# Performance work log

Measured on AMD Instinct MI355X. Metric: run time of the kernel, lower is better.

Reference implementation:

```python
import jax, jax.numpy as jnp
import numpy as np

B, D_IN, M, D_MEM = 65536, 64, 2048, 64


def setup_inputs() -> dict:
    key = jax.random.key(0)
    k = jax.random.split(key, 5)
    glorot = lambda kk, shape: jax.random.uniform(
        kk, shape, jnp.float32,
        -jnp.sqrt(6.0 / (shape[0] + shape[1])), jnp.sqrt(6.0 / (shape[0] + shape[1])))
    return {
        "inputs": jax.random.normal(k[0], (B, D_IN), jnp.float32),
        "W_att": glorot(k[1], (D_IN, M)),
        "b_att": jnp.zeros((M,), jnp.float32),
        "W_write": glorot(k[2], (D_IN, D_MEM)),
        "b_write": jnp.zeros((D_MEM,), jnp.float32),
        "memory": glorot(k[3], (M, D_MEM)),
        "update_gate": jnp.full((M,), 0.5, jnp.float32),
    }


def reference(inputs, W_att, b_att, W_write, b_write, memory, update_gate):
    # Read attention: Dense(memory_size, softmax) -> [B, M]
    read_attention = jax.nn.softmax(inputs @ W_att + b_att, axis=-1)
    # Read: [B, M] @ [M, Dm] -> [B, Dm]
    read_vector = read_attention @ memory
    # Write candidate: Dense(memory_dim, tanh) -> [B, Dm]
    candidate_write = jnp.tanh(inputs @ W_write + b_write)
    aggregated_write = jnp.mean(candidate_write, axis=0)[None, :]  # [1, Dm]
    write_attention = jnp.mean(read_attention, axis=0)             # [M]
    update_weights = (write_attention * update_gate)[:, None]      # [M, 1]
    # Gated in-place memory update (returned as new state)
    new_memory = memory * (1.0 - update_weights) + update_weights * aggregated_write
    return read_vector, new_memory
```

## Files before the change

### kernel.cpp

```cpp
#include <hip/hip_runtime.h>
#include <hip/hip_bf16.h>

typedef unsigned int   u32;
typedef unsigned short u16;

typedef __bf16 bf16x8 __attribute__((ext_vector_type(8)));
typedef float  f32x4  __attribute__((ext_vector_type(4)));
typedef u32    u32x4  __attribute__((ext_vector_type(4)));
typedef u32    u32x2  __attribute__((ext_vector_type(2)));

union Frag { u32x4 u; bf16x8 b; };

#define MFMA16 __builtin_amdgcn_mfma_f32_16x16x32_bf16

#define B_ROWS 65536
#define D_IN   64
#define M_SZ   2048
#define D_MEM  64

#define WT_OFF      0
#define MEMT_OFF    262144
#define WWT_OFF     524288
#define CSF_OFF     532480
#define AGF_OFF     540672
#define BATTS_OFF   540928

#define L2E 1.4426950408889634f

#define AS1 __attribute__((address_space(1)))
#define AS3 __attribute__((address_space(3)))

#if defined(__has_builtin)
#if __has_builtin(__builtin_amdgcn_global_load_lds)
#define HAS_GLD 1
#endif
#endif
#ifndef HAS_GLD
#define HAS_GLD 0
#endif

__device__ __forceinline__ float bf2f(u16 h) { return __uint_as_float(((u32)h) << 16); }
__device__ __forceinline__ u16 f2bf(float f) {
    u32 u = __float_as_uint(f);
    return (u16)((u + 0x7FFFu + ((u >> 16) & 1u)) >> 16);
}
#if defined(__has_builtin) && __has_builtin(__builtin_amdgcn_exp2f)
__device__ __forceinline__ float exp2fast(float x) { return __builtin_amdgcn_exp2f(x); }
#else
__device__ __forceinline__ float exp2fast(float x) { return __expf(x * 0.6931471805599453f); }
#endif
__device__ __forceinline__ float tanh_fast(float x) {
    const float e = exp2fast(x * (2.0f * L2E));
    return 1.0f - 2.0f * __builtin_amdgcn_rcpf(e + 1.0f);
}
__device__ __forceinline__ bool detect_bf16(const void* ug) {
    return ((const u32*)ug)[0] == 0x3F003F00u;
}
__device__ __forceinline__ float load_elem(const void* p, size_t i, bool isbf) {
    return isbf ? bf2f(((const u16*)p)[i]) : ((const float*)p)[i];
}

__device__ __forceinline__ u32 cvtpk_bf16(float lo, float hi) {
    u32 r;
    asm("v_cvt_pk_bf16_f32 %0, %1, %2" : "=v"(r) : "v"(lo), "v"(hi));
    return r;
}
#if defined(__has_builtin) && __has_builtin(__builtin_amdgcn_permlane32_swap) && \
    __has_builtin(__builtin_amdgcn_permlane16_swap)
__device__ __forceinline__ void pl32swap(u32& a, u32& b) {
    u32x2 r = __builtin_amdgcn_permlane32_swap(a, b, false, false);
    a = r[0]; b = r[1];
}
__device__ __forceinline__ void pl16swap(u32& a, u32& b) {
    u32x2 r = __builtin_amdgcn_permlane16_swap(a, b, false, false);
    a = r[0]; b = r[1];
}
#else
__device__ __forceinline__ void pl32swap(u32& a, u32& b) {
    asm("v_permlane32_swap_b32 %0, %1" : "+v"(a), "+v"(b));
}
__device__ __forceinline__ void pl16swap(u32& a, u32& b) {
    asm("v_permlane16_swap_b32 %0, %1" : "+v"(a), "+v"(b));
}
#endif
template<int CTRL>
__device__ __forceinline__ float xadd(float v) {
    int x = __builtin_amdgcn_update_dpp(0, __float_as_int(v), CTRL, 0xF, 0xF, true);
    return v + __int_as_float(x);
}

__global__ void __launch_bounds__(256)
prep_kernel(const void* Watt, const void* mem_in, const void* Wwr,
            const void* batt_in, const void* ug,
            u16* Wt, u16* memT, u16* Wwt, float* CSF, float* battS)
{
    const bool isbf = detect_bf16(ug);
    const int b = blockIdx.x;
    const int t = threadIdx.x;
    if (b == 65) {
        for (int i = t; i < 2112; i += 256) CSF[i] = 0.f;
        for (int i = t; i < 2048; i += 256)
            battS[i] = load_elem(batt_in, i, isbf) * L2E;
        return;
    }
    __shared__ u16 tile[64][65];
    const void* src; u16* dst; int C, rb, cb, bsel;
    if (b < 32)      { src = Watt;   dst = Wt;   C = 2048; rb = 0;           cb = b * 64; bsel = 0; }
    else if (b < 64) { src = mem_in; dst = memT; C = 64;   rb = (b-32) * 64; cb = 0;      bsel = 1; }
    else             { src = Wwr;    dst = Wwt;  C = 64;   rb = 0;           cb = 0;      bsel = 2; }

#pragma unroll
    for (int j = 0; j < 16; ++j) {
        int e = j * 256 + t;
        int r = e >> 6, c = e & 63;
        float v = load_elem(src, (size_t)(rb + r) * C + cb + c, isbf);
        tile[r][c] = f2bf(v);
    }
    __syncthreads();
#pragma unroll
    for (int j = 0; j < 16; ++j) {
        int e = j * 256 + t;
        int c2 = e >> 6, r2 = e & 63;
        size_t di;
        if (bsel == 0) {
            const int m = cb + c2;
            const int k2 = (r2 & 7) | ((((r2 >> 3) ^ m) & 7) << 3);
            di = (size_t)m * 64 + k2;
        } else if (bsel == 1) {
            const int m2 = (r2 & 7) | ((((r2 >> 3) ^ c2) & 7) << 3);
            di = (size_t)c2 * 2048 + rb + m2;
        } else {
            di = (size_t)c2 * 64 + r2;
        }
        dst[di] = tile[r2][c2];
    }
}

__global__ void __launch_bounds__(512, 4)
main_kernel(const void* x_in, const void* bwrite_in,
            const u16* __restrict__ Wt, const u16* __restrict__ memT,
            const u16* __restrict__ Wwt, const float* __restrict__ battS,
            const void* ug, float* CSF, float* AGF, void* out)
{
    const bool isbf = detect_bf16(ug);
    const int tid = threadIdx.x;
    const int lane = tid & 63, wave = tid >> 6;
    const int quad = lane >> 4, l4 = lane & 15;
    const int rowbase = blockIdx.x * 128;

    __shared__ __align__(16) u16 WtA[2][8192];
    __shared__ __align__(16) u16 MeL[2][64][128];
    __shared__ float csA[2112];

    const int wvu = __builtin_amdgcn_readfirstlane(wave);

    for (int i = tid; i < 2112; i += 512) csA[i] = 0.f;

    auto cp16 = [&](const char* gsrc_lane, char* lds_base_uniform) {
#if HAS_GLD
        __builtin_amdgcn_global_load_lds((const AS1 void*)gsrc_lane,
                                         (AS3 void*)lds_base_uniform, 16, 0, 0);
#else
        *(u32x4*)(lds_base_uniform + lane * 16) = *(const u32x4*)gsrc_lane;
#endif
    };
    auto stageWt = [&](int ch, int b) {
        char* lb = (char*)&WtA[b][0] + wvu * 2048;
        const char* gb = (const char*)Wt + (size_t)ch * 16384 + wvu * 2048 + lane * 16;
        cp16(gb, lb);
        cp16(gb + 1024, lb + 1024);
    };
    auto stageMe = [&](int ch, int b) {
#pragma unroll
        for (int j = 0; j < 2; ++j) {
            const int d = wvu * 8 + j * 4 + (lane >> 4);
            const char* gb = (const char*)memT + (size_t)d * 4096
                           + (size_t)ch * 256 + (lane & 15) * 16;
            char* lb = (char*)&MeL[b][wvu * 8 + j * 4][0];
            cp16(gb, lb);
        }
    };

    Frag a[2];
    {
        const int arow = rowbase + wave * 16 + l4;
        if (isbf) {
            const u16* xp = (const u16*)x_in + (size_t)arow * 64 + quad * 8;
            a[0].u = *(const u32x4*)xp;
            a[1].u = *(const u32x4*)(xp + 32);
        } else {
            const float* xp = (const float*)x_in + (size_t)arow * 64 + quad * 8;
#pragma unroll
            for (int j = 0; j < 8; ++j) {
                ((u16*)&a[0])[j] = f2bf(xp[j]);
                ((u16*)&a[1])[j] = f2bf(xp[32 + j]);
            }
        }
    }
    const f32x4 zf = {0.f, 0.f, 0.f, 0.f};

    stageWt(0, 0);

    float agout = 0.f;
    {
        f32x4 accW[4];
#pragma unroll
        for (int t = 0; t < 4; ++t) {
            const u16* bp = Wwt + (size_t)(t * 16 + l4) * 64 + quad * 8;
            Frag b0, b1; b0.u = *(const u32x4*)bp; b1.u = *(const u32x4*)(bp + 32);
            accW[t] = MFMA16(a[0].b, b0.b, zf, 0, 0, 0);
            accW[t] = MFMA16(a[1].b, b1.b, accW[t], 0, 0, 0);
        }
#pragma unroll
        for (int t = 0; t < 4; ++t) {
            const float bw = load_elem(bwrite_in, t * 16 + l4, isbf);
            float s = 0.f;
#pragma unroll
            for (int i = 0; i < 4; ++i) s += tanh_fast(accW[t][i] + bw);
            s += __shfl_xor(s, 16, 64);
            s += __shfl_xor(s, 32, 64);
            if (quad == t) agout = s;
        }
    }

    __syncthreads();
    atomicAdd(&csA[2048 + lane], agout);

    float lsum = 0.f;
    for (int ch = 0; ch < 16; ++ch) {
        const int cur = ch & 1;
        if (ch < 15) stageWt(ch + 1, cur ^ 1);
        for (int half = 0; half < 2; ++half) {
            const int mb = half * 64;
            const int mbase = ch * 128 + mb;
            Frag wb0[4], wb1[4]; f32x4 blv[4];
#pragma unroll
            for (int t = 0; t < 4; ++t) {
                const int rr = mb + t * 16 + l4, swr = rr & 7;
                wb0[t].u = *(const u32x4*)&WtA[cur][rr * 64 + ((quad ^ swr) << 3)];
                wb1[t].u = *(const u32x4*)&WtA[cur][rr * 64 + (((quad + 4) ^ swr) << 3)];
                blv[t] = *(const f32x4*)&battS[mbase + t * 16 + quad * 4];
            }
#pragma unroll
            for (int t = 0; t < 4; ++t) {
                f32x4 acc = MFMA16(wb0[t].b, a[0].b, zf, 0, 0, 0);
                acc = MFMA16(wb1[t].b, a[1].b, acc, 0, 0, 0);
#pragma unroll
                for (int i = 0; i < 4; ++i)
                    lsum += exp2fast(fmaf(acc[i], L2E, blv[t][i]));
            }
        }
        __syncthreads();
    }
    float invl;
    {
        float v = lsum;
        v += __shfl_xor(v, 16, 64);
        v += __shfl_xor(v, 32, 64);
        invl = 1.f / v;
    }

    f32x4 oaccT[4] = {zf, zf, zf, zf};
    stageMe(15, 1);
    __syncthreads();
    const bool sb0 = (l4 & 1), sb1 = (l4 & 2), sb2 = (l4 & 4), sb3 = (l4 & 8);
    for (int ch = 15; ch >= 0; --ch) {
        const int cur = ch & 1;
        if (ch > 0) { stageWt(ch - 1, cur ^ 1); stageMe(ch - 1, cur ^ 1); }
        for (int half = 0; half < 2; ++half) {
            const int mb = half * 64;
            const int mbase = ch * 128 + mb;
            const int mbh8 = mb >> 3;
            Frag wb0[4], wb1[4], mb0[4], mb1[4]; f32x4 blv[4];
#pragma unroll
            for (int t = 0; t < 4; ++t) {
                const int rr = mb + t * 16 + l4, swr = rr & 7;
                wb0[t].u = *(const u32x4*)&WtA[cur][rr * 64 + ((quad ^ swr) << 3)];
                wb1[t].u = *(const u32x4*)&WtA[cur][rr * 64 + (((quad + 4) ^ swr) << 3)];
                const int dd = t * 16 + l4, swd = dd & 7;
                mb0[t].u = *(const u32x4*)&MeL[cur][dd][(mbh8 | (quad ^ swd)) << 3];
                mb1[t].u = *(const u32x4*)&MeL[cur][dd][(mbh8 | ((quad + 4) ^ swd)) << 3];
                blv[t] = *(const f32x4*)&battS[mbase + t * 16 + quad * 4];
            }
            u32 P0[4], P1[4];
            float c16[16];
#pragma unroll
            for (int j = 0; j < 16; ++j) c16[j] = 0.f;
#pragma unroll
            for (int t = 0; t < 4; ++t) {
                f32x4 acc = MFMA16(wb0[t].b, a[0].b, zf, 0, 0, 0);
                acc = MFMA16(wb1[t].b, a[1].b, acc, 0, 0, 0);
                const float e0 = exp2fast(fmaf(acc[0], L2E, blv[t][0]));
                const float e1 = exp2fast(fmaf(acc[1], L2E, blv[t][1]));
                const float e2 = exp2fast(fmaf(acc[2], L2E, blv[t][2]));
                const float e3 = exp2fast(fmaf(acc[3], L2E, blv[t][3]));
                c16[t * 4 + 0] = fmaf(e0, invl, c16[t * 4 + 0]);
                c16[t * 4 + 1] = fmaf(e1, invl, c16[t * 4 + 1]);
                c16[t * 4 + 2] = fmaf(e2, invl, c16[t * 4 + 2]);
                c16[t * 4 + 3] = fmaf(e3, invl, c16[t * 4 + 3]);
                P0[t] = cvtpk_bf16(e0, e1);
                P1[t] = cvtpk_bf16(e2, e3);
            }
#pragma unroll
            for (int cc2 = 0; cc2 < 2; ++cc2) {
                u32 b0 = P0[2 * cc2], b2 = P0[2 * cc2 + 1];
                u32 b1 = P1[2 * cc2], b3 = P1[2 * cc2 + 1];
                pl32swap(b0, b2); pl16swap(b0, b2);
                pl32swap(b1, b3); pl16swap(b1, b3);
                Frag bf; bf.u = (u32x4){b0, b1, b2, b3};
#pragma unroll
                for (int dt = 0; dt < 4; ++dt) {
                    if (cc2 == 0)
                        oaccT[dt] = MFMA16(mb0[dt].b, bf.b, oaccT[dt], 0, 0, 0);
                    else
                        oaccT[dt] = MFMA16(mb1[dt].b, bf.b, oaccT[dt], 0, 0, 0);
                }
            }
            float u8[8];
#pragma unroll
            for (int k = 0; k < 8; ++k) {
                const float t0 = xadd<0xB1>(c16[2 * k]);
                const float t1 = xadd<0xB1>(c16[2 * k + 1]);
                u8[k] = sb0 ? t1 : t0;
            }
            float v4[4];
#pragma unroll
            for (int k = 0; k < 4; ++k) {
                const float t0 = xadd<0x4E>(u8[2 * k]);
                const float t1 = xadd<0x4E>(u8[2 * k + 1]);
                v4[k] = sb1 ? t1 : t0;
            }
            float w2[2];
#pragma unroll
            for (int k = 0; k < 2; ++k) {
                const float t0 = xadd<0x128>(v4[2 * k]);
                const float t1 = xadd<0x128>(v4[2 * k + 1]);
                w2[k] = sb3 ? t1 : t0;
            }
            const float f0 = w2[0] + __shfl_xor(w2[0], 4, 64);
            const float f1 = w2[1] + __shfl_xor(w2[1], 4, 64);
            const float csv = sb2 ? f1 : f0;
            const int tsel = ((l4 >> 3) & 1) | (((l4 >> 2) & 1) << 1);
            const int mout = mbase + tsel * 16 + quad * 4 + (l4 & 3);
            atomicAdd(&csA[mout], csv);
        }
        __syncthreads();
    }

    for (int i = tid; i < 2048; i += 512) atomicAdd(&CSF[i], csA[i]);
    if (tid < 64) atomicAdd(&AGF[tid], csA[2048 + tid]);

#pragma unroll
    for (int dt = 0; dt < 4; ++dt) {
        const int gr = rowbase + wave * 16 + l4;
        const int d0 = dt * 16 + quad * 4;
        const f32x4 o = oaccT[dt] * invl;
        if (isbf) {
            u32x2 w;
            w.x = cvtpk_bf16(o[0], o[1]);
            w.y = cvtpk_bf16(o[2], o[3]);
            *(u32x2*)&((u16*)out)[(size_t)gr * 64 + d0] = w;
        } else {
            *(f32x4*)&((float*)out)[(size_t)gr * 64 + d0] = o;
        }
    }
}

__global__ void __launch_bounds__(256)
finalize_kernel(const void* mem_in, const void* ug,
                const float* __restrict__ CSF, const float* __restrict__ AGF,
                void* out)
{
    const bool isbf = detect_bf16(ug);
    const int idx = blockIdx.x * 256 + threadIdx.x;
    const int m = idx >> 6, d = idx & 63;
    const float wa  = CSF[m] * (1.f / 65536.f);
    const float agg = AGF[d] * (1.f / 65536.f);
    const float uw  = wa * load_elem(ug, m, isbf);
    const float mv  = load_elem(mem_in, idx, isbf);
    const float nm  = mv * (1.f - uw) + uw * agg;
    if (isbf) ((u16*)out)[(size_t)4194304 + idx] = f2bf(nm);
    else      ((float*)out)[(size_t)4194304 + idx] = nm;
}

extern "C" void kernel_launch(void* const* d_in, const int* in_sizes, int n_in,
                              void* d_out, int out_size, void* d_ws, size_t ws_size,
                              hipStream_t stream)
{
    (void)in_sizes; (void)n_in; (void)out_size; (void)ws_size;
    const void* x    = d_in[0];
    const void* Watt = d_in[1];
    const void* batt = d_in[2];
    const void* Wwr  = d_in[3];
    const void* bwr  = d_in[4];
    const void* mem  = d_in[5];
    const void* ug   = d_in[6];

    char* ws = (char*)d_ws;
    u16*   Wt    = (u16*)(ws + WT_OFF);
    u16*   memT  = (u16*)(ws + MEMT_OFF);
    u16*   Wwt   = (u16*)(ws + WWT_OFF);
    float* CSF   = (float*)(ws + CSF_OFF);
    float* AGF   = (float*)(ws + AGF_OFF);
    float* battS = (float*)(ws + BATTS_OFF);

    prep_kernel<<<66, 256, 0, stream>>>(Watt, mem, Wwr, batt, ug,
                                        Wt, memT, Wwt, CSF, battS);
    main_kernel<<<512, 512, 0, stream>>>(x, bwr, Wt, memT, Wwt, battS, ug,
                                         CSF, AGF, d_out);
    finalize_kernel<<<512, 256, 0, stream>>>(mem, ug, CSF, AGF, d_out);
}
```

Measured before the change: 203.5 us.

## Process four row groups per wave to reuse staged weight and memory tiles

Each wave now handles 64 input rows (four 16-row groups) instead of 16, so every Wt and memT fragment read from LDS feeds four times as many MFMAs. The launch shrinks to 256 blocks of 256 threads, each covering 256 rows. This halves the global staging traffic per row and amortizes LDS reads, but it multiplies register use (oaccT grows from 4 to 16 accumulators, plus the extra A fragments), drops occupancy to one block per CU, and leaves only 256 blocks on a 256-CU device, so latency hiding may suffer.

```diff
diff --git a/kernel.cpp b/kernel.cpp
--- a/kernel.cpp
+++ b/kernel.cpp
@@ -136,7 +136,7 @@
     }
 }
 
-__global__ void __launch_bounds__(512, 4)
+__global__ void __launch_bounds__(256, 1)
 main_kernel(const void* x_in, const void* bwrite_in,
             const u16* __restrict__ Wt, const u16* __restrict__ memT,
             const u16* __restrict__ Wwt, const float* __restrict__ battS,
@@ -146,7 +146,7 @@
     const int tid = threadIdx.x;
     const int lane = tid & 63, wave = tid >> 6;
     const int quad = lane >> 4, l4 = lane & 15;
-    const int rowbase = blockIdx.x * 128;
+    const int rowbase = blockIdx.x * 256;
 
     __shared__ __align__(16) u16 WtA[2][8192];
     __shared__ __align__(16) u16 MeL[2][64][128];
@@ -154,7 +154,7 @@
 
     const int wvu = __builtin_amdgcn_readfirstlane(wave);
 
-    for (int i = tid; i < 2112; i += 512) csA[i] = 0.f;
+    for (int i = tid; i < 2112; i += 256) csA[i] = 0.f;
 
     auto cp16 = [&](const char* gsrc_lane, char* lds_base_uniform) {
 #if HAS_GLD
@@ -165,35 +165,37 @@
 #endif
     };
     auto stageWt = [&](int ch, int b) {
-        char* lb = (char*)&WtA[b][0] + wvu * 2048;
-        const char* gb = (const char*)Wt + (size_t)ch * 16384 + wvu * 2048 + lane * 16;
-        cp16(gb, lb);
-        cp16(gb + 1024, lb + 1024);
+        char* lb = (char*)&WtA[b][0] + wvu * 4096;
+        const char* gb = (const char*)Wt + (size_t)ch * 16384 + wvu * 4096 + lane * 16;
+#pragma unroll
+        for (int j = 0; j < 4; ++j)
+            cp16(gb + j * 1024, lb + j * 1024);
     };
     auto stageMe = [&](int ch, int b) {
 #pragma unroll
-        for (int j = 0; j < 2; ++j) {
-            const int d = wvu * 8 + j * 4 + (lane >> 4);
+        for (int j = 0; j < 4; ++j) {
+            const int d = wvu * 16 + j * 4 + (lane >> 4);
             const char* gb = (const char*)memT + (size_t)d * 4096
                            + (size_t)ch * 256 + (lane & 15) * 16;
-            char* lb = (char*)&MeL[b][wvu * 8 + j * 4][0];
+            char* lb = (char*)&MeL[b][wvu * 16 + j * 4][0];
             cp16(gb, lb);
         }
     };
 
-    Frag a[2];
-    {
-        const int arow = rowbase + wave * 16 + l4;
+    Frag a[4][2];
+#pragma unroll
+    for (int rg = 0; rg < 4; ++rg) {
+        const int arow = rowbase + wave * 64 + rg * 16 + l4;
         if (isbf) {
             const u16* xp = (const u16*)x_in + (size_t)arow * 64 + quad * 8;
-            a[0].u = *(const u32x4*)xp;
-            a[1].u = *(const u32x4*)(xp + 32);
+            a[rg][0].u = *(const u32x4*)xp;
+            a[rg][1].u = *(const u32x4*)(xp + 32);
         } else {
             const float* xp = (const float*)x_in + (size_t)arow * 64 + quad * 8;
 #pragma unroll
             for (int j = 0; j < 8; ++j) {
-                ((u16*)&a[0])[j] = f2bf(xp[j]);
-                ((u16*)&a[1])[j] = f2bf(xp[32 + j]);
+                ((u16*)&a[rg][0])[j] = f2bf(xp[j]);
+                ((u16*)&a[rg][1])[j] = f2bf(xp[32 + j]);
             }
         }
     }
@@ -203,20 +205,19 @@
 
     float agout = 0.f;
     {
-        f32x4 accW[4];
 #pragma unroll
         for (int t = 0; t < 4; ++t) {
             const u16* bp = Wwt + (size_t)(t * 16 + l4) * 64 + quad * 8;
             Frag b0, b1; b0.u = *(const u32x4*)bp; b1.u = *(const u32x4*)(bp + 32);
-            accW[t] = MFMA16(a[0].b, b0.b, zf, 0, 0, 0);
-            accW[t] = MFMA16(a[1].b, b1.b, accW[t], 0, 0, 0);
-        }
-#pragma unroll
-        for (int t = 0; t < 4; ++t) {
             const float bw = load_elem(bwrite_in, t * 16 + l4, isbf);
             float s = 0.f;
 #pragma unroll
-            for (int i = 0; i < 4; ++i) s += tanh_fast(accW[t][i] + bw);
+            for (int rg = 0; rg < 4; ++rg) {
+                f32x4 acc = MFMA16(a[rg][0].b, b0.b, zf, 0, 0, 0);
+                acc = MFMA16(a[rg][1].b, b1.b, acc, 0, 0, 0);
+#pragma unroll
+                for (int i = 0; i < 4; ++i) s += tanh_fast(acc[i] + bw);
+            }
             s += __shfl_xor(s, 16, 64);
             s += __shfl_xor(s, 32, 64);
             if (quad == t) agout = s;
@@ -226,7 +227,7 @@
     __syncthreads();
     atomicAdd(&csA[2048 + lane], agout);
 
-    float lsum = 0.f;
+    float lsum[4] = {0.f, 0.f, 0.f, 0.f};
     for (int ch = 0; ch < 16; ++ch) {
         const int cur = ch & 1;
         if (ch < 15) stageWt(ch + 1, cur ^ 1);
@@ -242,25 +243,28 @@
                 blv[t] = *(const f32x4*)&battS[mbase + t * 16 + quad * 4];
             }
 #pragma unroll
-            for (int t = 0; t < 4; ++t) {
-                f32x4 acc = MFMA16(wb0[t].b, a[0].b, zf, 0, 0, 0);
-                acc = MFMA16(wb1[t].b, a[1].b, acc, 0, 0, 0);
-#pragma unroll
-                for (int i = 0; i < 4; ++i)
-                    lsum += exp2fast(fmaf(acc[i], L2E, blv[t][i]));
-            }
+            for (int rg = 0; rg < 4; ++rg)
+#pragma unroll
+                for (int t = 0; t < 4; ++t) {
+                    f32x4 acc = MFMA16(wb0[t].b, a[rg][0].b, zf, 0, 0, 0);
+                    acc = MFMA16(wb1[t].b, a[rg][1].b, acc, 0, 0, 0);
+#pragma unroll
+                    for (int i = 0; i < 4; ++i)
+                        lsum[rg] += exp2fast(fmaf(acc[i], L2E, blv[t][i]));
+                }
         }
         __syncthreads();
     }
-    float invl;
-    {
-        float v = lsum;
+    float invl[4];
+#pragma unroll
+    for (int rg = 0; rg < 4; ++rg) {
+        float v = lsum[rg];
         v += __shfl_xor(v, 16, 64);
         v += __shfl_xor(v, 32, 64);
-        invl = 1.f / v;
-    }
-
-    f32x4 oaccT[4] = {zf, zf, zf, zf};
+        invl[rg] = 1.f / v;
+    }
+
+    f32x4 oaccT[4][4] = {{zf,zf,zf,zf},{zf,zf,zf,zf},{zf,zf,zf,zf},{zf,zf,zf,zf}};
     stageMe(15, 1);
     __syncthreads();
     const bool sb0 = (l4 & 1), sb1 = (l4 & 2), sb2 = (l4 & 4), sb3 = (l4 & 8);
@@ -282,38 +286,42 @@
                 mb1[t].u = *(const u32x4*)&MeL[cur][dd][(mbh8 | ((quad + 4) ^ swd)) << 3];
                 blv[t] = *(const f32x4*)&battS[mbase + t * 16 + quad * 4];
             }
-            u32 P0[4], P1[4];
             float c16[16];
 #pragma unroll
             for (int j = 0; j < 16; ++j) c16[j] = 0.f;
 #pragma unroll
-            for (int t = 0; t < 4; ++t) {
-                f32x4 acc = MFMA16(wb0[t].b, a[0].b, zf, 0, 0, 0);
-                acc = MFMA16(wb1[t].b, a[1].b, acc, 0, 0, 0);
-                const float e0 = exp2fast(fmaf(acc[0], L2E, blv[t][0]));
-                const float e1 = exp2fast(fmaf(acc[1], L2E, blv[t][1]));
-                const float e2 = exp2fast(fmaf(acc[2], L2E, blv[t][2]));
-                const float e3 = exp2fast(fmaf(acc[3], L2E, blv[t][3]));
-                c16[t * 4 + 0] = fmaf(e0, invl, c16[t * 4 + 0]);
-                c16[t * 4 + 1] = fmaf(e1, invl, c16[t * 4 + 1]);
-                c16[t * 4 + 2] = fmaf(e2, invl, c16[t * 4 + 2]);
-                c16[t * 4 + 3] = fmaf(e3, invl, c16[t * 4 + 3]);
-                P0[t] = cvtpk_bf16(e0, e1);
-                P1[t] = cvtpk_bf16(e2, e3);
-            }
-#pragma unroll
-            for (int cc2 = 0; cc2 < 2; ++cc2) {
-                u32 b0 = P0[2 * cc2], b2 = P0[2 * cc2 + 1];
-                u32 b1 = P1[2 * cc2], b3 = P1[2 * cc2 + 1];
-                pl32swap(b0, b2); pl16swap(b0, b2);
-                pl32swap(b1, b3); pl16swap(b1, b3);
-                Frag bf; bf.u = (u32x4){b0, b1, b2, b3};
-#pragma unroll
-                for (int dt = 0; dt < 4; ++dt) {
-                    if (cc2 == 0)
-                        oaccT[dt] = MFMA16(mb0[dt].b, bf.b, oaccT[dt], 0, 0, 0);
-                    else
-                        oaccT[dt] = MFMA16(mb1[dt].b, bf.b, oaccT[dt], 0, 0, 0);
+            for (int rg = 0; rg < 4; ++rg) {
+                u32 P0[4], P1[4];
+                const float il = invl[rg];
+#pragma unroll
+                for (int t = 0; t < 4; ++t) {
+                    f32x4 acc = MFMA16(wb0[t].b, a[rg][0].b, zf, 0, 0, 0);
+                    acc = MFMA16(wb1[t].b, a[rg][1].b, acc, 0, 0, 0);
+                    const float e0 = exp2fast(fmaf(acc[0], L2E, blv[t][0]));
+                    const float e1 = exp2fast(fmaf(acc[1], L2E, blv[t][1]));
+                    const float e2 = exp2fast(fmaf(acc[2], L2E, blv[t][2]));
+                    const float e3 = exp2fast(fmaf(acc[3], L2E, blv[t][3]));
+                    c16[t * 4 + 0] = fmaf(e0, il, c16[t * 4 + 0]);
+                    c16[t * 4 + 1] = fmaf(e1, il, c16[t * 4 + 1]);
+                    c16[t * 4 + 2] = fmaf(e2, il, c16[t * 4 + 2]);
+                    c16[t * 4 + 3] = fmaf(e3, il, c16[t * 4 + 3]);
+                    P0[t] = cvtpk_bf16(e0, e1);
+                    P1[t] = cvtpk_bf16(e2, e3);
+                }
+#pragma unroll
+                for (int cc2 = 0; cc2 < 2; ++cc2) {
+                    u32 b0 = P0[2 * cc2], b2 = P0[2 * cc2 + 1];
+                    u32 b1 = P1[2 * cc2], b3 = P1[2 * cc2 + 1];
+                    pl32swap(b0, b2); pl16swap(b0, b2);
+                    pl32swap(b1, b3); pl16swap(b1, b3);
+                    Frag bf; bf.u = (u32x4){b0, b1, b2, b3};
+#pragma unroll
+                    for (int dt = 0; dt < 4; ++dt) {
+                        if (cc2 == 0)
+                            oaccT[rg][dt] = MFMA16(mb0[dt].b, bf.b, oaccT[rg][dt], 0, 0, 0);
+                        else
+                            oaccT[rg][dt] = MFMA16(mb1[dt].b, bf.b, oaccT[rg][dt], 0, 0, 0);
+                    }
                 }
             }
             float u8[8];
@@ -347,23 +355,25 @@
         __syncthreads();
     }
 
-    for (int i = tid; i < 2048; i += 512) atomicAdd(&CSF[i], csA[i]);
+    for (int i = tid; i < 2048; i += 256) atomicAdd(&CSF[i], csA[i]);
     if (tid < 64) atomicAdd(&AGF[tid], csA[2048 + tid]);
 
 #pragma unroll
-    for (int dt = 0; dt < 4; ++dt) {
-        const int gr = rowbase + wave * 16 + l4;
-        const int d0 = dt * 16 + quad * 4;
-        const f32x4 o = oaccT[dt] * invl;
-        if (isbf) {
-            u32x2 w;
-            w.x = cvtpk_bf16(o[0], o[1]);
-            w.y = cvtpk_bf16(o[2], o[3]);
-            *(u32x2*)&((u16*)out)[(size_t)gr * 64 + d0] = w;
-        } else {
-            *(f32x4*)&((float*)out)[(size_t)gr * 64 + d0] = o;
-        }
-    }
+    for (int rg = 0; rg < 4; ++rg)
+#pragma unroll
+        for (int dt = 0; dt < 4; ++dt) {
+            const int gr = rowbase + wave * 64 + rg * 16 + l4;
+            const int d0 = dt * 16 + quad * 4;
+            const f32x4 o = oaccT[rg][dt] * invl[rg];
+            if (isbf) {
+                u32x2 w;
+                w.x = cvtpk_bf16(o[0], o[1]);
+                w.y = cvtpk_bf16(o[2], o[3]);
+                *(u32x2*)&((u16*)out)[(size_t)gr * 64 + d0] = w;
+            } else {
+                *(f32x4*)&((float*)out)[(size_t)gr * 64 + d0] = o;
+            }
+        }
 }
 
 __global__ void __launch_bounds__(256)
@@ -406,7 +416,7 @@
 
     prep_kernel<<<66, 256, 0, stream>>>(Watt, mem, Wwr, batt, ug,
                                         Wt, memT, Wwt, CSF, battS);
-    main_kernel<<<512, 512, 0, stream>>>(x, bwr, Wt, memT, Wwt, battS, ug,
+    main_kernel<<<256, 256, 0, stream>>>(x, bwr, Wt, memT, Wwt, battS, ug,
                                          CSF, AGF, d_out);
     finalize_kernel<<<512, 256, 0, stream>>>(mem, ug, CSF, AGF, d_out);
 }
```

Result: faster. 197.3 us (-3.0%).
